# Kernel tuning notes

Hardware: AMD Instinct MI355X
Metric: run time of the kernel (lower is better)

## Reference

```python
import jax, jax.numpy as jnp
import numpy as np

B, L = 128, 64000
FS, STEP, NFILT, HID, HID2, OUT = 256, 200, 64, 512, 512, 10


def _ilin(lb, ub, W, b=0.0):
    # interval affine: center/radius form
    c = (lb + ub) * 0.5
    r = (ub - lb) * 0.5
    oc = c @ W + b
    orr = r @ jnp.abs(W)
    return oc - orr, oc + orr


def _imul(al, au, bl, bu):
    # interval product: extremes over 4 corner products
    p = jnp.stack([al * bl, al * bu, au * bl, au * bu])
    return p.min(axis=0), p.max(axis=0)


def _cell(xl, xu, hl, hu, cl, cu, wih, whh, bias):
    # interval LSTM cell, torch gate order i,f,g,o
    gl1, gu1 = _ilin(xl, xu, wih)
    gl2, gu2 = _ilin(hl, hu, whh)
    gl = gl1 + gl2 + bias
    gu = gu1 + gu2 + bias
    il, fl, ggl, ol = jnp.split(gl, 4, axis=-1)
    iu, fu, ggu, ou = jnp.split(gu, 4, axis=-1)
    il, iu = jax.nn.sigmoid(il), jax.nn.sigmoid(iu)
    fl, fu = jax.nn.sigmoid(fl), jax.nn.sigmoid(fu)
    ggl, ggu = jnp.tanh(ggl), jnp.tanh(ggu)
    fcl, fcu = _imul(fl, fu, cl, cu)
    igl, igu = _imul(il, iu, ggl, ggu)
    ncl, ncu = fcl + igl, fcu + igu
    nhl, nhu = _imul(jax.nn.sigmoid(ol), jax.nn.sigmoid(ou), jnp.tanh(ncl), jnp.tanh(ncu))
    return nhl, nhu, ncl, ncu


def setup_inputs() -> dict:
    key = jax.random.key(0)
    ks = jax.random.split(key, 13)
    x = 0.1 * jax.random.normal(ks[0], (B, L), jnp.float32)
    eps = 0.01
    s = 0.3  # keep LSTM gates out of saturation
    return {
        "input_lb": x - eps,
        "input_ub": x + eps,
        "mtx1": jax.random.normal(ks[1], (FS, FS + 2), jnp.float32) / np.float32(np.sqrt(FS)),
        "mtx2": jax.random.uniform(ks[2], (FS + 2, NFILT), jnp.float32) / np.float32(FS + 2),
        "lin1_w": jax.random.normal(ks[3], (NFILT, HID), jnp.float32) / np.float32(np.sqrt(NFILT)),
        "lin1_b": 0.01 * jax.random.normal(ks[4], (HID,), jnp.float32),
        "w_ih0": s * jax.random.normal(ks[5], (HID, 4 * HID2), jnp.float32) / np.float32(np.sqrt(HID)),
        "w_hh0": s * jax.random.normal(ks[6], (HID2, 4 * HID2), jnp.float32) / np.float32(np.sqrt(HID2)),
        "b0": 0.01 * jax.random.normal(ks[7], (4 * HID2,), jnp.float32),
        "w_ih1": s * jax.random.normal(ks[8], (HID2, 4 * HID2), jnp.float32) / np.float32(np.sqrt(HID2)),
        "w_hh1": s * jax.random.normal(ks[9], (HID2, 4 * HID2), jnp.float32) / np.float32(np.sqrt(HID2)),
        "b1": 0.01 * jax.random.normal(ks[10], (4 * HID2,), jnp.float32),
        "lin2_w": jax.random.normal(ks[11], (HID2, OUT), jnp.float32) / np.float32(np.sqrt(HID2)),
        "lin2_b": 0.01 * jax.random.normal(ks[12], (OUT,), jnp.float32),
    }


def reference(input_lb, input_ub, mtx1, mtx2, lin1_w, lin1_b,
              w_ih0, w_hh0, b0, w_ih1, w_hh1, b1, lin2_w, lin2_b):
    Bc, Lc = input_lb.shape
    pad = jnp.zeros((Bc, STEP), input_lb.dtype)
    lb = jnp.concatenate([input_lb, pad], axis=1)
    ub = jnp.concatenate([input_ub, pad], axis=1)
    Lp = Lc + STEP
    F = (Lp - FS - 1) // STEP + 1  # frames with i + FS < Lp (break condition)
    idx = jnp.arange(F)[:, None] * STEP + jnp.arange(FS)[None, :]  # [F, FS]
    flb, fub = lb[:, idx], ub[:, idx]  # [B, F, FS]
    # pre-LSTM interval chain, vectorized over all frames
    l1l, l1u = _ilin(flb, fub, mtx1)  # [B, F, FS+2]
    a, b = l1l * l1l, l1u * l1u
    squ = jnp.maximum(a, b)
    sql = jnp.where((l1l <= 0) & (l1u >= 0), 0.0, jnp.minimum(a, b))
    l2l, l2u = _ilin(sql, squ, mtx2, 1e-10)  # mtx2 >= 0, inputs >= 0 -> lb > 0
    lgl, lgu = jnp.log(l2l), jnp.log(l2u)
    n1l, n1u = _ilin(lgl, lgu, lin1_w, lin1_b)  # [B, F, HID]
    rl, ru = jnp.maximum(n1l, 0.0), jnp.maximum(n1u, 0.0)

    H2 = w_hh0.shape[0]
    z = jnp.zeros((Bc, H2), input_lb.dtype)

    def step(carry, xs):
        h0l, h0u, c0l, c0u, h1l, h1u, c1l, c1u = carry
        xl, xu = xs
        h0l, h0u, c0l, c0u = _cell(xl, xu, h0l, h0u, c0l, c0u, w_ih0, w_hh0, b0)
        h1l, h1u, c1l, c1u = _cell(h0l, h0u, h1l, h1u, c1l, c1u, w_ih1, w_hh1, b1)
        return (h0l, h0u, c0l, c0u, h1l, h1u, c1l, c1u), None

    carry, _ = jax.lax.scan(step, (z,) * 8,
                            (jnp.swapaxes(rl, 0, 1), jnp.swapaxes(ru, 0, 1)))
    h1l, h1u = carry[4], carry[5]  # last frame, top LSTM layer
    ol, ou = _ilin(h1l, h1u, lin2_w, lin2_b)
    return jnp.stack([ol, ou])  # [2, B, OUT] logit bounds
```

## Files before the change

### kernel.cpp

```cpp
#include <hip/hip_runtime.h>
#include <hip/hip_bf16.h>
#include <math.h>

#define BATCH 128
#define LEN   64000
#define FS    256
#define STEPS 200
#define NFILT 64
#define HID   512
#define HID2  512
#define NOUT  10
#define NF    320
#define G4    2048
#define KTOT  1024
#define NBLK  256
#define HSLOT (BATCH * HID2)

typedef __bf16  bf16x8 __attribute__((ext_vector_type(8)));
typedef float   f32x4  __attribute__((ext_vector_type(4)));
typedef __hip_bfloat16 hbf;
typedef unsigned long long ull;

#define ARV(b)  (128 + (b) * 16)
#define REL_(i) (128 + 4096 + (i) * 16)
#define BAR_WORDS (128 + 4096 + 128)

__device__ __forceinline__ float fsig(float x) { return 1.f / (1.f + __expf(-x)); }
__device__ __forceinline__ float ftanh(float x) { return 1.f - 2.f / (__expf(2.f * x) + 1.f); }
__device__ __forceinline__ void imulf_(float al, float au, float bl, float bu,
                                       float& lo, float& hi) {
    const float p1 = al * bl, p2 = al * bu, p3 = au * bl, p4 = au * bu;
    lo = fminf(fminf(p1, p2), fminf(p3, p4));
    hi = fmaxf(fmaxf(p1, p2), fmaxf(p3, p4));
}

__device__ __forceinline__ bf16x8 loadA16_agent(const hbf* p) {
    union { ull u[2]; bf16x8 v; } t;
    ull* q = (ull*)p;
    t.u[0] = __hip_atomic_load(q,     __ATOMIC_RELAXED, __HIP_MEMORY_SCOPE_AGENT);
    t.u[1] = __hip_atomic_load(q + 1, __ATOMIC_RELAXED, __HIP_MEMORY_SCOPE_AGENT);
    return t.v;
}
__device__ __forceinline__ unsigned ld_flag(const unsigned* p) {
    return __hip_atomic_load(p, __ATOMIC_RELAXED, __HIP_MEMORY_SCOPE_AGENT);
}
__device__ __forceinline__ void st_flag(unsigned* p, unsigned v) {
    __hip_atomic_store(p, v, __ATOMIC_RELAXED, __HIP_MEMORY_SCOPE_AGENT);
}

__global__ __launch_bounds__(256) void prep_weights_kernel(
    const float* __restrict__ wih, const float* __restrict__ whh,
    hbf* __restrict__ Wt)
{
    __shared__ float tile[32][33];
    const int n0 = blockIdx.x * 32;
    const int k0 = blockIdx.y * 32;
    const int tx = threadIdx.x & 31;
    const int ty = threadIdx.x >> 5;

    for (int r = ty; r < 32; r += 8) {
        const int k = k0 + r;
        const float* src = (k < HID) ? (wih + (size_t)k * G4)
                                     : (whh + (size_t)(k - HID) * G4);
        tile[r][tx] = src[n0 + tx];
    }
    __syncthreads();
    for (int r = ty; r < 32; r += 8) {
        const int n = n0 + r;
        Wt[(size_t)n * KTOT + k0 + tx] = __float2bfloat16(tile[tx][r]);
    }
}

__global__ __launch_bounds__(256) void prep_mtx1_kernel(
    const float* __restrict__ mtx1, hbf* __restrict__ W)
{
    __shared__ float tile[32][33];
    const int n0 = blockIdx.x * 32;
    const int k0 = blockIdx.y * 32;
    const int tx = threadIdx.x & 31;
    const int ty = threadIdx.x >> 5;

    for (int r = ty; r < 32; r += 8) {
        const int k = k0 + r;
        const int n = n0 + tx;
        tile[r][tx] = (n < FS + 2) ? mtx1[k * (FS + 2) + n] : 0.f;
    }
    __syncthreads();
    for (int r = ty; r < 32; r += 8) {
        const int n = n0 + r;
        if (n < 272)
            W[(size_t)n * 256 + k0 + tx] = __float2bfloat16(tile[tx][r]);
    }
}

__global__ __launch_bounds__(256) void prep_lin1_kernel(
    const float* __restrict__ lin1_w, hbf* __restrict__ W)
{
    __shared__ float tile[32][33];
    const int n0 = blockIdx.x * 32;
    const int k0 = blockIdx.y * 32;
    const int tx = threadIdx.x & 31;
    const int ty = threadIdx.x >> 5;

    for (int r = ty; r < 32; r += 8)
        tile[r][tx] = lin1_w[(size_t)(k0 + r) * HID + n0 + tx];
    __syncthreads();
    for (int r = ty; r < 32; r += 8)
        W[(size_t)(n0 + r) * 64 + k0 + tx] = __float2bfloat16(tile[tx][r]);
}

#define FB_A1C  0
#define FB_A1R  8704
#define FB_O1C  17408
#define FB_O1R  34816
#define FB_S3C  52224
#define FB_S3R  54272
#define FB_SIZE 56320

__global__ __launch_bounds__(512) void frontend3_kernel(
    const float* __restrict__ lb, const float* __restrict__ ub,
    const hbf* __restrict__ Wt1f,
    const float* __restrict__ mtx2,
    const hbf* __restrict__ Wt3f,
    const float* __restrict__ lin1_b,
    hbf* __restrict__ Xc, hbf* __restrict__ Xr)
{
    __shared__ char fbuf[FB_SIZE];
    hbf*   A1c = (hbf*)(fbuf + FB_A1C);
    hbf*   A1r = (hbf*)(fbuf + FB_A1R);
    float* o1C = (float*)(fbuf + FB_O1C);
    float* o1R = (float*)(fbuf + FB_O1R);
    hbf*   SQL = A1c;
    hbf*   SQU = A1r;
    hbf*   s3c = (hbf*)(fbuf + FB_S3C);
    hbf*   s3r = (hbf*)(fbuf + FB_S3R);

    const int tid  = threadIdx.x;
    const int row0 = blockIdx.x * 16;
    const int b    = row0 / NF;
    const int f0   = row0 % NF;

    for (int c = tid; c < 16 * 256; c += 512) {
        const int m = c >> 8, i = c & 255;
        const int pos = (f0 + m) * STEPS + i;
        float l = 0.f, u = 0.f;
        if (pos < LEN) {
            l = lb[(size_t)b * LEN + pos];
            u = ub[(size_t)b * LEN + pos];
        }
        A1c[m * 272 + i] = __float2bfloat16(0.5f * (l + u));
        A1r[m * 272 + i] = __float2bfloat16(0.5f * (u - l));
    }
    __syncthreads();

    {
        const int w    = tid >> 6;
        const int lane = tid & 63;
        const int op   = w & 1;
        const int nh   = w >> 1;
        const int rc   = lane & 15;
        const int gk   = lane >> 4;
        const unsigned amask = op ? 0x7FFF7FFFu : 0xFFFFFFFFu;
        const hbf* ap = (op ? A1r : A1c) + rc * 272 + 8 * gk;
        float* outp = op ? o1R : o1C;
        const int nt0 = nh * 4, nt1 = (nh == 3) ? 17 : nh * 4 + 4;

        for (int nt = nt0; nt < nt1; ++nt) {
            f32x4 acc = {0.f, 0.f, 0.f, 0.f};
            const hbf* bp = Wt1f + (size_t)(nt * 16 + rc) * 256 + 8 * gk;
#pragma unroll
            for (int k0 = 0; k0 < 256; k0 += 32) {
                const bf16x8 afr = *(const bf16x8*)(ap + k0);
                union { bf16x8 v; unsigned u[4]; } t2;
                t2.v = *(const bf16x8*)(bp + k0);
                t2.u[0] &= amask; t2.u[1] &= amask;
                t2.u[2] &= amask; t2.u[3] &= amask;
                acc = __builtin_amdgcn_mfma_f32_16x16x32_bf16(afr, t2.v, acc, 0, 0, 0);
            }
            const int n = nt * 16 + rc;
#pragma unroll
            for (int reg = 0; reg < 4; ++reg)
                outp[(4 * gk + reg) * 272 + n] = acc[reg];
        }
    }
    __syncthreads();

    for (int c = tid; c < 16 * 258; c += 512) {
        const int m = c / 258, n = c - m * 258;
        const float oc = o1C[m * 272 + n];
        const float orr = o1R[m * 272 + n];
        const float l1l = oc - orr, l1u = oc + orr;
        const float a = l1l * l1l, bb = l1u * l1u;
        const float squ = fmaxf(a, bb);
        const float sql = (l1l <= 0.f && l1u >= 0.f) ? 0.f : fminf(a, bb);
        SQL[m * 272 + n] = __float2bfloat16(sql);
        SQU[m * 272 + n] = __float2bfloat16(squ);
    }
    __syncthreads();

    for (int idx = tid; idx < 16 * 64; idx += 512) {
        const int m = idx >> 6, n = idx & 63;
        float l2l = 1e-10f, l2u = 1e-10f;
#pragma unroll 2
        for (int i = 0; i < 258; ++i) {
            const float w = mtx2[i * NFILT + n];
            l2l = fmaf(__bfloat162float(SQL[m * 272 + i]), w, l2l);
            l2u = fmaf(__bfloat162float(SQU[m * 272 + i]), w, l2u);
        }
        const float lgl = logf(l2l);
        const float lgu = logf(l2u);
        s3c[m * 64 + n] = __float2bfloat16(0.5f * (lgl + lgu));
        s3r[m * 64 + n] = __float2bfloat16(0.5f * (lgu - lgl));
    }
    __syncthreads();

    {
        const int w    = tid >> 6;
        const int lane = tid & 63;
        const int rc   = lane & 15;
        const int gk   = lane >> 4;
        const hbf* apc = s3c + rc * 64 + 8 * gk;
        const hbf* apr = s3r + rc * 64 + 8 * gk;

        for (int nt = w * 4; nt < w * 4 + 4; ++nt) {
            f32x4 accC = {0.f, 0.f, 0.f, 0.f};
            f32x4 accR = {0.f, 0.f, 0.f, 0.f};
            const hbf* bp = Wt3f + (size_t)(nt * 16 + rc) * 64 + 8 * gk;
#pragma unroll
            for (int k0 = 0; k0 < 64; k0 += 32) {
                const bf16x8 ac = *(const bf16x8*)(apc + k0);
                const bf16x8 ar = *(const bf16x8*)(apr + k0);
                union { bf16x8 v; unsigned u[4]; } tw, ta;
                tw.v = *(const bf16x8*)(bp + k0);
                ta.v = tw.v;
                ta.u[0] &= 0x7FFF7FFFu; ta.u[1] &= 0x7FFF7FFFu;
                ta.u[2] &= 0x7FFF7FFFu; ta.u[3] &= 0x7FFF7FFFu;
                accC = __builtin_amdgcn_mfma_f32_16x16x32_bf16(ac, tw.v, accC, 0, 0, 0);
                accR = __builtin_amdgcn_mfma_f32_16x16x32_bf16(ar, ta.v, accR, 0, 0, 0);
            }
            const int n = nt * 16 + rc;
            const float bn = lin1_b[n];
#pragma unroll
            for (int reg = 0; reg < 4; ++reg) {
                const int m = 4 * gk + reg;
                const float oc = accC[reg] + bn;
                const float orr = accR[reg];
                const float n1l = oc - orr, n1u = oc + orr;
                const float rl = fmaxf(n1l, 0.f), ru = fmaxf(n1u, 0.f);
                const size_t o = ((size_t)(f0 + m) * BATCH + b) * HID + n;
                Xc[o] = __float2bfloat16(0.5f * (rl + ru));
                Xr[o] = __float2bfloat16(0.5f * (ru - rl));
            }
        }
    }
}

__device__ __forceinline__ void gbar(unsigned* bar, unsigned gen,
                                     int bid, int tid) {
    __builtin_amdgcn_s_waitcnt(0);
    __syncthreads();
    if (bid == 0) {
        if (tid != 0) {
            while (ld_flag(&bar[ARV(tid)]) < gen)
                __builtin_amdgcn_s_sleep(1);
        }
        __syncthreads();
        if (tid < 8) st_flag(&bar[REL_(tid)], gen);
    } else {
        if (tid == 0) {
            st_flag(&bar[ARV(bid)], gen);
            while (ld_flag(&bar[REL_(bid & 7)]) < gen)
                __builtin_amdgcn_s_sleep(4);
        }
        asm volatile("" ::: "memory");
    }
    __syncthreads();
}

__device__ __forceinline__ void cell_elem(
    const float C[4], const float R[4], const float bs[4],
    float& cl_r, float& cu_r, float& nhl, float& nhu)
{
    float gl[4], gu[4];
#pragma unroll
    for (int g = 0; g < 4; ++g) {
        gl[g] = C[g] - R[g] + bs[g];
        gu[g] = C[g] + R[g] + bs[g];
    }
    const float il = fsig(gl[0]), iu = fsig(gu[0]);
    const float fl = fsig(gl[1]), fu = fsig(gu[1]);
    const float ggl = ftanh(gl[2]), ggu = ftanh(gu[2]);
    const float ol = fsig(gl[3]), ou = fsig(gu[3]);

    float fcl, fcu, igl, igu;
    imulf_(fl, fu, cl_r, cu_r, fcl, fcu);
    imulf_(il, iu, ggl, ggu, igl, igu);
    const float ncl = fcl + igl, ncu = fcu + igu;
    cl_r = ncl; cu_r = ncu;
    imulf_(ol, ou, ftanh(ncl), ftanh(ncu), nhl, nhu);
}

#define GEMM_HALF(KBASE, MASKED)                                               \
    _Pragma("unroll")                                                          \
    for (int kk = 0; kk < 16; ++kk) {                                          \
        const int KK = (KBASE) + kk;                                           \
        _Pragma("unroll")                                                      \
        for (int g = 0; g < 4; ++g) {                                          \
            union { bf16x8 v; unsigned u[4]; } t2;                             \
            t2.v = *(const bf16x8*)&Wlds[(size_t)(((g << 5) | KK) * 64 + lane) * 8]; \
            if (MASKED) {                                                      \
                t2.u[0] &= 0x7FFF7FFFu; t2.u[1] &= 0x7FFF7FFFu;                \
                t2.u[2] &= 0x7FFF7FFFu; t2.u[3] &= 0x7FFF7FFFu;                \
            }                                                                  \
            acc[g] = __builtin_amdgcn_mfma_f32_16x16x32_bf16(af[kk], t2.v, acc[g], 0, 0, 0); \
        }                                                                      \
    }

#define LOADA16(PTR)                                                           \
    _Pragma("unroll")                                                          \
    for (int i = 0; i < 16; ++i) af[i] = *(const bf16x8*)((PTR) + 32 * i);

#define POLL_CNT(GID, TGT)                                                     \
    if (tid == 0) {                                                            \
        const unsigned* pp = &gcnt[(GID) * 16];                                \
        while ((int)ld_flag(pp) < (TGT)) __builtin_amdgcn_s_sleep(1);          \
    }                                                                          \
    __syncthreads();

__global__ __launch_bounds__(256, 1) void lstm_persistent(
    const hbf* Xc, const hbf* Xr,
    hbf* Ring1C, hbf* Ring1R,
    const hbf* __restrict__ Wt0, const hbf* __restrict__ Wt1,
    const float* __restrict__ b0, const float* __restrict__ b1,
    hbf* __restrict__ Ring0C, hbf* __restrict__ Ring0R,
    hbf* __restrict__ RP0C, hbf* __restrict__ RP0R,
    int useP0,
    const hbf* __restrict__ Zbuf,
    hbf* __restrict__ H1c0, hbf* __restrict__ H1r0,
    hbf* __restrict__ H1c1, hbf* __restrict__ H1r1,
    float* __restrict__ h1l, float* __restrict__ h1u,
    unsigned* __restrict__ bar, unsigned* __restrict__ tkt,
    unsigned* __restrict__ gcnt)
{
    const int tid = threadIdx.x;
    const int bid = blockIdx.x;

    __shared__ unsigned s_info, s_map;
    __shared__ int s_fast;
    __shared__ hbf   Wlds[4 * 32 * 64 * 8];
    __shared__ float red[2][2][4][64][4];
    __shared__ unsigned short houtC[32][16], houtR[32][16];

    if (tid == 0) {
        unsigned xcc;
        asm volatile("s_getreg_b32 %0, hwreg(HW_REG_XCC_ID)" : "=s"(xcc));
        xcc &= 7u;
        const unsigned slot = __hip_atomic_fetch_add(
            &tkt[xcc * 16], 1u, __ATOMIC_RELAXED, __HIP_MEMORY_SCOPE_AGENT);
        s_info = (xcc << 16) | slot;
    }
    gbar(bar, 1, bid, tid);
    if (tid == 0) {
        unsigned cnt[8]; bool ok = true;
        for (int y = 0; y < 8; ++y) {
            cnt[y] = ld_flag(&tkt[y * 16]);
            ok = ok && (cnt[y] == 32u);
        }
        const unsigned xcc = s_info >> 16, slot = s_info & 0xffffu;
        unsigned rank;
        if (ok) rank = xcc * 32u + slot;
        else { rank = slot; for (unsigned y = 0; y < xcc; ++y) rank += cnt[y]; }
        s_map = rank; s_fast = ok ? 1 : 0;
    }
    __syncthreads();

    const unsigned rank = s_map;
    const bool fast = (s_fast != 0);
    int layer, mgrp, jslot;
    if (fast) { layer = (rank >> 5) & 1; mgrp = rank >> 6; jslot = rank & 31; }
    else      { layer = rank >> 7; mgrp = (rank >> 5) & 3; jslot = rank & 31; }
    const int m0 = mgrp * 32;
    const int j0 = jslot * 16;
    const int gid  = layer * 4 + mgrp;
    const int pgid = mgrp;
    const bool p0 = fast && (useP0 != 0);

    {
        const hbf* Wt = layer ? Wt1 : Wt0;
        for (int c = tid; c < 8192; c += 256) {
            const int g  = c >> 11;
            const int kk = (c >> 6) & 31;
            const int l6 = c & 63;
            const int n  = g * HID2 + j0 + (l6 & 15);
            const int k  = kk * 32 + (l6 >> 4) * 8;
            *(ulonglong2*)&Wlds[(size_t)c * 8] =
                *(const ulonglong2*)(Wt + (size_t)n * KTOT + k);
        }
    }

    const int w    = tid >> 6;
    const int lane = tid & 63;
    const int op   = w & 1;
    const int mh   = w >> 1;
    const int rc   = lane & 15;
    const int gk   = lane >> 4;
    const int aoff = (m0 + mh * 16 + rc) * 512 + 8 * gk;

    hbf* H1cb[2] = { H1c0, H1c1 };
    hbf* H1rb[2] = { H1r0, H1r1 };

    const int mm  = tid >> 4;
    const int cj  = tid & 15;
    const int ll  = ((mm >> 2) << 4) | cj;
    const int rr  = mm & 3;
    const int idx0 = (m0 + mm) * HID2 + j0 + cj;
    const int idx1 = idx0 + 16 * HID2;
    const float* bias = layer ? b1 : b0;
    float bs[4];
#pragma unroll
    for (int g = 0; g < 4; ++g) bs[g] = bias[g * HID2 + j0 + cj];

    const int st_arr = tid >> 7;
    const int st_row = (tid >> 2) & 31;
    const int st_q   = tid & 3;
    const size_t st_off = (size_t)(m0 + st_row) * 512 + j0 + st_q * 4;

    float cAl = 0.f, cAu = 0.f, cBl = 0.f, cBu = 0.f;

    __syncthreads();

    bf16x8 xf[16];
    if (layer == 0) {
        const hbf* p = (op ? Xr : Xc) + aoff;
        bf16x8* af = xf;
        LOADA16(p)
    }

    for (int t = 0; t < NF; ++t) {
        const int wslot = t & 1, rslot = wslot ^ 1;
        f32x4 acc[4] = {f32x4{0,0,0,0}, f32x4{0,0,0,0},
                        f32x4{0,0,0,0}, f32x4{0,0,0,0}};

        if (layer == 0) {
            {
                bf16x8* af = xf;
                if (op) { GEMM_HALF(0, 1) } else { GEMM_HALF(0, 0) }
                const int tn = (t + 1 < NF) ? (t + 1) : t;
                const hbf* p = (op ? Xr : Xc) + (size_t)tn * HSLOT + aoff;
                LOADA16(p)
            }
            POLL_CNT(gid, 32 * t)
            {
                const hbf* p;
                if (t == 0)       p = Zbuf + aoff;
                else if (p0)      p = (op ? RP0R : RP0C) + (size_t)(t - 1) * HSLOT + aoff;
                else              p = (op ? Ring0R : Ring0C) + (size_t)(t - 1) * HSLOT + aoff;
                bf16x8 af[16];
                LOADA16(p)
                if (op) { GEMM_HALF(16, 1) } else { GEMM_HALF(16, 0) }
            }
        } else {
            POLL_CNT(gid, 32 * t)
            {
                bf16x8 af[16];
                if (fast) {
                    const hbf* p = (t == 0) ? (Zbuf + aoff)
                        : ((op ? (const hbf*)Ring1R : (const hbf*)Ring1C)
                           + (size_t)(t - 1) * HSLOT + aoff);
                    LOADA16(p)
                } else {
                    const hbf* p = (op ? H1rb[rslot] : H1cb[rslot]) + aoff;
#pragma unroll
                    for (int i = 0; i < 16; ++i) af[i] = loadA16_agent(p + 32 * i);
                }
                if (op) { GEMM_HALF(16, 1) } else { GEMM_HALF(16, 0) }
            }
            POLL_CNT(pgid, 32 * (t + 1))
            {
                const hbf* p = (op ? Ring0R : Ring0C) + (size_t)t * HSLOT + aoff;
                bf16x8 af[16];
                LOADA16(p)
                if (op) { GEMM_HALF(0, 1) } else { GEMM_HALF(0, 0) }
            }
        }

#pragma unroll
        for (int g = 0; g < 4; ++g)
            *((f32x4*)&red[op][mh][g][lane][0]) = acc[g];
        __syncthreads();

        {
            float C0[4], R0[4], C1[4], R1[4];
#pragma unroll
            for (int g = 0; g < 4; ++g) {
                C0[g] = red[0][0][g][ll][rr];
                R0[g] = red[1][0][g][ll][rr];
                C1[g] = red[0][1][g][ll][rr];
                R1[g] = red[1][1][g][ll][rr];
            }
            const bool writeF = (layer == 1) && (t == NF - 1);

            float nhl, nhu;
            cell_elem(C0, R0, bs, cAl, cAu, nhl, nhu);
            {
                const __hip_bfloat16 hc = __float2bfloat16(0.5f * (nhl + nhu));
                const __hip_bfloat16 hr = __float2bfloat16(0.5f * (nhu - nhl));
                houtC[mm][cj] = *(const unsigned short*)&hc;
                houtR[mm][cj] = *(const unsigned short*)&hr;
            }
            if (writeF) { h1l[idx0] = nhl; h1u[idx0] = nhu; }

            cell_elem(C1, R1, bs, cBl, cBu, nhl, nhu);
            {
                const __hip_bfloat16 hc = __float2bfloat16(0.5f * (nhl + nhu));
                const __hip_bfloat16 hr = __float2bfloat16(0.5f * (nhu - nhl));
                houtC[mm + 16][cj] = *(const unsigned short*)&hc;
                houtR[mm + 16][cj] = *(const unsigned short*)&hr;
            }
            if (writeF) { h1l[idx1] = nhl; h1u[idx1] = nhu; }
        }
        __syncthreads();

        {
            const ull v = *(const ull*)
                &(st_arr ? houtR : houtC)[st_row][st_q * 4];
            if (layer == 0) {
                hbf* aC = Ring0C + (size_t)t * HSLOT;
                hbf* aR = Ring0R + (size_t)t * HSLOT;
                __hip_atomic_store((ull*)((st_arr ? aR : aC) + st_off), v,
                                   __ATOMIC_RELAXED, __HIP_MEMORY_SCOPE_AGENT);
                if (p0) {
                    hbf* pC = RP0C + (size_t)t * HSLOT;
                    hbf* pR = RP0R + (size_t)t * HSLOT;
                    *(ull*)((st_arr ? pR : pC) + st_off) = v;
                }
            } else if (fast) {
                hbf* pC = Ring1C + (size_t)t * HSLOT;
                hbf* pR = Ring1R + (size_t)t * HSLOT;
                *(ull*)((st_arr ? pR : pC) + st_off) = v;
            } else {
                hbf* dC = H1cb[wslot];
                hbf* dR = H1rb[wslot];
                __hip_atomic_store((ull*)((st_arr ? dR : dC) + st_off), v,
                                   __ATOMIC_RELAXED, __HIP_MEMORY_SCOPE_AGENT);
            }
        }

        __builtin_amdgcn_s_waitcnt(0);
        __syncthreads();
        if (tid == 0)
            __hip_atomic_fetch_add(&gcnt[gid * 16], 1u, __ATOMIC_RELAXED,
                                   __HIP_MEMORY_SCOPE_AGENT);
    }
}

__global__ __launch_bounds__(64) void final_kernel(
    const float* __restrict__ h1l, const float* __restrict__ h1u,
    const float* __restrict__ w, const float* __restrict__ bias,
    float* __restrict__ out)
{
    const int b = blockIdx.x;
    const int j = threadIdx.x;
    if (j < NOUT) {
        float oc = bias[j], orr = 0.f;
        for (int i = 0; i < HID2; ++i) {
            const float lo = h1l[(size_t)b * HID2 + i];
            const float hi = h1u[(size_t)b * HID2 + i];
            const float wv = w[i * NOUT + j];
            oc  = fmaf(0.5f * (lo + hi), wv, oc);
            orr = fmaf(0.5f * (hi - lo), fabsf(wv), orr);
        }
        out[b * NOUT + j] = oc - orr;
        out[BATCH * NOUT + b * NOUT + j] = oc + orr;
    }
}

extern "C" void kernel_launch(void* const* d_in, const int* in_sizes, int n_in,
                              void* d_out, int out_size, void* d_ws, size_t ws_size,
                              hipStream_t stream)
{
    const float* input_lb = (const float*)d_in[0];
    const float* input_ub = (const float*)d_in[1];
    const float* mtx1     = (const float*)d_in[2];
    const float* mtx2     = (const float*)d_in[3];
    const float* lin1_w   = (const float*)d_in[4];
    const float* lin1_b   = (const float*)d_in[5];
    const float* w_ih0    = (const float*)d_in[6];
    const float* w_hh0    = (const float*)d_in[7];
    const float* b0       = (const float*)d_in[8];
    const float* w_ih1    = (const float*)d_in[9];
    const float* w_hh1    = (const float*)d_in[10];
    const float* b1       = (const float*)d_in[11];
    const float* lin2_w   = (const float*)d_in[12];
    const float* lin2_b   = (const float*)d_in[13];
    float* out = (float*)d_out;

    char* ws = (char*)d_ws;
    size_t off = 0;
    hbf* Xc = (hbf*)(ws + off); off += (size_t)NF * HSLOT * 2;
    hbf* Xr = (hbf*)(ws + off); off += (size_t)NF * HSLOT * 2;
    hbf* Wt0 = (hbf*)(ws + off); off += (size_t)G4 * KTOT * 2;
    hbf* Wt1 = (hbf*)(ws + off); off += (size_t)G4 * KTOT * 2;
    hbf* Wt1f = (hbf*)(ws + off); off += (size_t)272 * 256 * 2;
    hbf* Wt3f = (hbf*)(ws + off); off += (size_t)512 * 64 * 2;
    hbf* Ring0C = (hbf*)(ws + off); off += (size_t)NF * HSLOT * 2;
    hbf* Ring0R = (hbf*)(ws + off); off += (size_t)NF * HSLOT * 2;

    char* zbase = ws + off;
    hbf* Zbuf = (hbf*)(ws + off); off += (size_t)HSLOT * 2;
    hbf* H1c0 = (hbf*)(ws + off); off += (size_t)HSLOT * 2;
    hbf* H1r0 = (hbf*)(ws + off); off += (size_t)HSLOT * 2;
    hbf* H1c1 = (hbf*)(ws + off); off += (size_t)HSLOT * 2;
    hbf* H1r1 = (hbf*)(ws + off); off += (size_t)HSLOT * 2;
    unsigned* tkt  = (unsigned*)(ws + off); off += (size_t)8 * 16 * 4;
    unsigned* bar  = (unsigned*)(ws + off); off += (size_t)BAR_WORDS * 4;
    unsigned* gcnt = (unsigned*)(ws + off); off += (size_t)8 * 16 * 4;
    const size_t zbytes = (size_t)((ws + off) - zbase);
    float* h1l = (float*)(ws + off); off += (size_t)HSLOT * 4;
    float* h1u = (float*)(ws + off); off += (size_t)HSLOT * 4;

    hbf* RP0C = Ring0C;
    hbf* RP0R = Ring0R;
    int useP0 = 0;
    {
        const size_t need = (size_t)NF * HSLOT * 2 * 2;
        if (off + need <= ws_size) {
            RP0C = (hbf*)(ws + off); off += (size_t)NF * HSLOT * 2;
            RP0R = (hbf*)(ws + off); off += (size_t)NF * HSLOT * 2;
            useP0 = 1;
        }
    }

    hipMemsetAsync(zbase, 0, zbytes, stream);

    {
        const dim3 pgrid(G4 / 32, KTOT / 32);
        prep_weights_kernel<<<pgrid, 256, 0, stream>>>(w_ih0, w_hh0, Wt0);
        prep_weights_kernel<<<pgrid, 256, 0, stream>>>(w_ih1, w_hh1, Wt1);
        prep_mtx1_kernel<<<dim3(9, 8), 256, 0, stream>>>(mtx1, Wt1f);
        prep_lin1_kernel<<<dim3(16, 2), 256, 0, stream>>>(lin1_w, Wt3f);
    }

    frontend3_kernel<<<(BATCH * NF) / 16, 512, 0, stream>>>(
        input_lb, input_ub, Wt1f, mtx2, Wt3f, lin1_b, Xc, Xr);

    lstm_persistent<<<NBLK, 256, 0, stream>>>(
        Xc, Xr, Xc, Xr, Wt0, Wt1, b0, b1,
        Ring0C, Ring0R, RP0C, RP0R, useP0, Zbuf,
        H1c0, H1r0, H1c1, H1r1,
        h1l, h1u, bar, tkt, gcnt);

    final_kernel<<<BATCH, 64, 0, stream>>>(h1l, h1u, lin2_w, lin2_b, out);
}
```

Before: 2.794 ms.

## Poll XCC-local step counters and defer cross-die layer-0 output publication

Adds a second counter array that is bumped with workgroup-scope atomics, and has same-group polling spin mostly on it, checking the agent-scope global counter only every sixteenth spin. When the private layer-0 ring is in use, the agent-scope store of layer-0 hidden state for layer 1 is deferred by one step and issued at the start of the next step, overlapping it with the input GEMM. Layer 1's cross wait now targets one extra step, and a tail store plus counter bump publishes the final frame. The aim is to cut cross-XCC coherence latency on the recurrent critical path. The cost is extra atomics per step, and it relies on workgroup-scope atomics being visible across blocks on the same die, which is a memory-ordering risk.

```diff
diff --git a/kernel.cpp b/kernel.cpp
--- a/kernel.cpp
+++ b/kernel.cpp
@@ -46,6 +46,14 @@
 }
 __device__ __forceinline__ void st_flag(unsigned* p, unsigned v) {
     __hip_atomic_store(p, v, __ATOMIC_RELAXED, __HIP_MEMORY_SCOPE_AGENT);
+}
+__device__ __forceinline__ unsigned rd_cnt_local(unsigned* p) {
+    return __hip_atomic_fetch_add(p, 0u, __ATOMIC_RELAXED,
+                                  __HIP_MEMORY_SCOPE_WORKGROUP);
+}
+__device__ __forceinline__ void bump_local(unsigned* p) {
+    __hip_atomic_fetch_add(p, 1u, __ATOMIC_RELAXED,
+                           __HIP_MEMORY_SCOPE_WORKGROUP);
 }
 
 __global__ __launch_bounds__(256) void prep_weights_kernel(
@@ -320,7 +328,20 @@
     _Pragma("unroll")                                                          \
     for (int i = 0; i < 16; ++i) af[i] = *(const bf16x8*)((PTR) + 32 * i);
 
-#define POLL_CNT(GID, TGT)                                                     \
+#define POLL_OWN(GID, TGT)                                                     \
+    if (tid == 0) {                                                            \
+        unsigned* lp = &lcnt[(GID) * 16];                                      \
+        const unsigned* gp = &gcnt[(GID) * 16];                                \
+        int spins = 0;                                                         \
+        for (;;) {                                                             \
+            if ((int)rd_cnt_local(lp) >= (TGT)) break;                         \
+            if (((++spins) & 15) == 0 && (int)ld_flag(gp) >= (TGT)) break;     \
+            __builtin_amdgcn_s_sleep(1);                                       \
+        }                                                                      \
+    }                                                                          \
+    __syncthreads();
+
+#define POLL_CROSS(GID, TGT)                                                   \
     if (tid == 0) {                                                            \
         const unsigned* pp = &gcnt[(GID) * 16];                                \
         while ((int)ld_flag(pp) < (TGT)) __builtin_amdgcn_s_sleep(1);          \
@@ -340,7 +361,7 @@
     hbf* __restrict__ H1c1, hbf* __restrict__ H1r1,
     float* __restrict__ h1l, float* __restrict__ h1u,
     unsigned* __restrict__ bar, unsigned* __restrict__ tkt,
-    unsigned* __restrict__ gcnt)
+    unsigned* __restrict__ gcnt, unsigned* __restrict__ lcnt)
 {
     const int tid = threadIdx.x;
     const int bid = blockIdx.x;
@@ -442,6 +463,14 @@
                         f32x4{0,0,0,0}, f32x4{0,0,0,0}};
 
         if (layer == 0) {
+            if (p0 && t > 0) {
+                const ull v = *(const ull*)
+                    &(st_arr ? houtR : houtC)[st_row][st_q * 4];
+                hbf* aC = Ring0C + (size_t)(t - 1) * HSLOT;
+                hbf* aR = Ring0R + (size_t)(t - 1) * HSLOT;
+                __hip_atomic_store((ull*)((st_arr ? aR : aC) + st_off), v,
+                                   __ATOMIC_RELAXED, __HIP_MEMORY_SCOPE_AGENT);
+            }
             {
                 bf16x8* af = xf;
                 if (op) { GEMM_HALF(0, 1) } else { GEMM_HALF(0, 0) }
@@ -449,7 +478,7 @@
                 const hbf* p = (op ? Xr : Xc) + (size_t)tn * HSLOT + aoff;
                 LOADA16(p)
             }
-            POLL_CNT(gid, 32 * t)
+            POLL_OWN(gid, 32 * t)
             {
                 const hbf* p;
                 if (t == 0)       p = Zbuf + aoff;
@@ -460,7 +489,7 @@
                 if (op) { GEMM_HALF(16, 1) } else { GEMM_HALF(16, 0) }
             }
         } else {
-            POLL_CNT(gid, 32 * t)
+            POLL_OWN(gid, 32 * t)
             {
                 bf16x8 af[16];
                 if (fast) {
@@ -475,7 +504,7 @@
                 }
                 if (op) { GEMM_HALF(16, 1) } else { GEMM_HALF(16, 0) }
             }
-            POLL_CNT(pgid, 32 * (t + 1))
+            POLL_CROSS(pgid, 32 * (t + (p0 ? 2 : 1)))
             {
                 const hbf* p = (op ? Ring0R : Ring0C) + (size_t)t * HSLOT + aoff;
                 bf16x8 af[16];
@@ -525,14 +554,15 @@
             const ull v = *(const ull*)
                 &(st_arr ? houtR : houtC)[st_row][st_q * 4];
             if (layer == 0) {
-                hbf* aC = Ring0C + (size_t)t * HSLOT;
-                hbf* aR = Ring0R + (size_t)t * HSLOT;
-                __hip_atomic_store((ull*)((st_arr ? aR : aC) + st_off), v,
-                                   __ATOMIC_RELAXED, __HIP_MEMORY_SCOPE_AGENT);
                 if (p0) {
                     hbf* pC = RP0C + (size_t)t * HSLOT;
                     hbf* pR = RP0R + (size_t)t * HSLOT;
                     *(ull*)((st_arr ? pR : pC) + st_off) = v;
+                } else {
+                    hbf* aC = Ring0C + (size_t)t * HSLOT;
+                    hbf* aR = Ring0R + (size_t)t * HSLOT;
+                    __hip_atomic_store((ull*)((st_arr ? aR : aC) + st_off), v,
+                                       __ATOMIC_RELAXED, __HIP_MEMORY_SCOPE_AGENT);
                 }
             } else if (fast) {
                 hbf* pC = Ring1C + (size_t)t * HSLOT;
@@ -546,6 +576,22 @@
             }
         }
 
+        __builtin_amdgcn_s_waitcnt(0);
+        __syncthreads();
+        if (tid == 0) {
+            bump_local(&lcnt[gid * 16]);
+            __hip_atomic_fetch_add(&gcnt[gid * 16], 1u, __ATOMIC_RELAXED,
+                                   __HIP_MEMORY_SCOPE_AGENT);
+        }
+    }
+
+    if (layer == 0 && p0) {
+        const ull v = *(const ull*)
+            &(st_arr ? houtR : houtC)[st_row][st_q * 4];
+        hbf* aC = Ring0C + (size_t)(NF - 1) * HSLOT;
+        hbf* aR = Ring0R + (size_t)(NF - 1) * HSLOT;
+        __hip_atomic_store((ull*)((st_arr ? aR : aC) + st_off), v,
+                           __ATOMIC_RELAXED, __HIP_MEMORY_SCOPE_AGENT);
         __builtin_amdgcn_s_waitcnt(0);
         __syncthreads();
         if (tid == 0)
@@ -615,6 +661,7 @@
     unsigned* tkt  = (unsigned*)(ws + off); off += (size_t)8 * 16 * 4;
     unsigned* bar  = (unsigned*)(ws + off); off += (size_t)BAR_WORDS * 4;
     unsigned* gcnt = (unsigned*)(ws + off); off += (size_t)8 * 16 * 4;
+    unsigned* lcnt = (unsigned*)(ws + off); off += (size_t)8 * 16 * 4;
     const size_t zbytes = (size_t)((ws + off) - zbase);
     float* h1l = (float*)(ws + off); off += (size_t)HSLOT * 4;
     float* h1u = (float*)(ws + off); off += (size_t)HSLOT * 4;
@@ -648,7 +695,7 @@
         Xc, Xr, Xc, Xr, Wt0, Wt1, b0, b1,
         Ring0C, Ring0R, RP0C, RP0R, useP0, Zbuf,
         H1c0, H1r0, H1c1, H1r1,
-        h1l, h1u, bar, tkt, gcnt);
+        h1l, h1u, bar, tkt, gcnt, lcnt);
 
     final_kernel<<<BATCH, 64, 0, stream>>>(h1l, h1u, lin2_w, lin2_b, out);
 }
```

New measurement: 3.338 ms. +19.4%, slower.
